# Kernel optimization log

Measured on AMD Instinct MI355X. Metric: run time of the kernel, lower is better.

## Reference

```python
import jax, jax.numpy as jnp
import numpy as np

B = 1024      # batch
D = 512       # input/output dim per module
H = 1024      # expert hidden dim
T = 8         # num_tasks
NTE = 2       # experts per task
NSE = 2       # shared experts
E = T * NTE + NSE   # 18 experts per layer
# expert_input_idx: each expert reads the module it belongs to (tasks 0..7, shared=8)
EXPERT_IDX = np.array([m for m in range(T + 1) for _ in range(2)])  # [E]


def _lin_init(k, shape, fan_in):
    s = 1.0 / np.sqrt(fan_in)
    return jax.random.uniform(k, shape, jnp.float32, -s, s)


def setup_inputs() -> dict:
    key = jax.random.key(0)
    ks = jax.random.split(key, 20)
    inp = {"inputs": jax.random.normal(ks[0], (B, T + 1, D), jnp.float32)}
    # layer 0: experts D->H->D (stacked over E), gates for M=9 modules
    inp["W1_0"] = _lin_init(ks[1], (E, D, H), D)
    inp["b1_0"] = _lin_init(ks[2], (E, H), D)
    inp["W2_0"] = _lin_init(ks[3], (E, H, D), H)
    inp["b2_0"] = _lin_init(ks[4], (E, D), H)
    inp["Wg_0"] = _lin_init(ks[5], (T + 1, D, E), D)
    inp["bg_0"] = _lin_init(ks[6], (T + 1, E), D)
    # layer 1 (final): gates only for M=T modules
    inp["W1_1"] = _lin_init(ks[7], (E, D, H), D)
    inp["b1_1"] = _lin_init(ks[8], (E, H), D)
    inp["W2_1"] = _lin_init(ks[9], (E, H, D), H)
    inp["b2_1"] = _lin_init(ks[10], (E, D), H)
    inp["Wg_1"] = _lin_init(ks[11], (T, D, E), D)
    inp["bg_1"] = _lin_init(ks[12], (T, E), D)
    # self-exp residual weights: per task [L=2, NTE], shared [L-1=1, NSE]
    sc = 1.0 / np.sqrt(NTE)
    inp["sew_task"] = jax.random.uniform(ks[13], (T, 2, NTE), jnp.float32, -sc, sc)
    inp["sew_shared"] = jax.random.uniform(ks[14], (1, NSE), jnp.float32, -sc, sc)
    return inp


def _build_add(rows):
    # rows: list of [2]-vectors, one per fully-active module; block-diagonal layout
    M = len(rows)
    add = jnp.zeros((M, E), jnp.float32)
    for m, w in enumerate(rows):
        add = add.at[m, 2 * m:2 * m + 2].set(w)
    return add


def _layer(x, W1, b1, W2, b2, Wg, bg, add):
    # x: [B, M_in, D]; experts share input of their owning module
    xe = x[:, EXPERT_IDX, :]                                   # [B, E, D]
    h = jax.nn.relu(jnp.einsum('bed,edh->beh', xe, W1) + b1)   # [B, E, H]
    eo = jnp.einsum('beh,eho->beo', h, W2) + b2                # [B, E, D]
    M = Wg.shape[0]
    g = jax.nn.softmax(jnp.einsum('bmd,mde->bme', x[:, :M, :], Wg) + bg, axis=-1)
    g = g + add[None]                                          # self-exp residual
    return jnp.einsum('bme,beo->bmo', g, eo)                   # [B, M, D]


def reference(inputs, W1_0, b1_0, W2_0, b2_0, Wg_0, bg_0,
              W1_1, b1_1, W2_1, b2_1, Wg_1, bg_1, sew_task, sew_shared):
    add0 = _build_add([sew_task[t, 0] for t in range(T)] + [sew_shared[0]])  # [T+1, E]
    add1 = _build_add([sew_task[t, 1] for t in range(T)])                    # [T, E]
    x = _layer(inputs, W1_0, b1_0, W2_0, b2_0, Wg_0, bg_0, add0)  # [B, T+1, D]
    x = _layer(x, W1_1, b1_1, W2_1, b2_1, Wg_1, bg_1, add1)       # [B, T, D]
    return x
```

## Files before the change

kernel.cpp:

```cpp
#include <hip/hip_runtime.h>

typedef unsigned short u16;
typedef unsigned int u32;
typedef __attribute__((ext_vector_type(8))) short short8;
typedef __attribute__((ext_vector_type(4))) float floatx4;

#define GLOAD_LDS16(gp, lp)                                                              \
  __builtin_amdgcn_global_load_lds((const __attribute__((address_space(1))) void*)(gp),  \
                                   (__attribute__((address_space(3))) void*)(lp), 16, 0, 0)

__device__ __forceinline__ u16 f2bf(float f) {
  u32 u = __float_as_uint(f);
  u += 0x7fffu + ((u >> 16) & 1u);
  return (u16)(u >> 16);
}

__device__ __forceinline__ void bf8_to_f(const u16* p, float* o) {
  const uint4 v = *(const uint4*)p;
  const u32 a[4] = {v.x, v.y, v.z, v.w};
#pragma unroll
  for (int i = 0; i < 4; i++) {
    o[2 * i]     = __uint_as_float(a[i] << 16);
    o[2 * i + 1] = __uint_as_float(a[i] & 0xffff0000u);
  }
}

__global__ __launch_bounds__(256) void prep_kernel(
    const float* __restrict__ W1a, const float* __restrict__ W2a,
    const float* __restrict__ W1b, const float* __restrict__ W2b,
    u16* __restrict__ T1a, u16* __restrict__ T2a,
    u16* __restrict__ T1b, u16* __restrict__ T2b,
    const float* __restrict__ Wg0, const float* __restrict__ Wg1,
    u16* __restrict__ WgT0, u16* __restrict__ WgT1,
    const float* __restrict__ x0, u16* __restrict__ x0bf) {
  __shared__ float tile[64][65];
  const int id = blockIdx.x;
  const int t = threadIdx.x;

  if (id < 9216) {
    const int tsel = id / 2304;
    const int rem = id % 2304;
    const int e = rem >> 7;
    const int t128 = rem & 127;
    const int K = (tsel & 1) ? 1024 : 512;
    const int N = (tsel & 1) ? 512 : 1024;
    const int kt = (tsel & 1) ? (t128 & 15) : (t128 & 7);
    const int nt = (tsel & 1) ? (t128 >> 4) : (t128 >> 3);
    const int k0 = kt * 64, n0 = nt * 64;
    const float* W = (tsel == 0) ? W1a : (tsel == 1) ? W2a : (tsel == 2) ? W1b : W2b;
    u16* WT = (tsel == 0) ? T1a : (tsel == 1) ? T2a : (tsel == 2) ? T1b : T2b;

    const float* Wp = W + ((size_t)e * K + k0) * N + n0;
    const int r = t >> 4;
    const int c = (t & 15) << 2;
#pragma unroll
    for (int p = 0; p < 4; p++) {
      const int row = r + p * 16;
      const float4 v = *(const float4*)(Wp + (size_t)row * N + c);
      tile[row][c + 0] = v.x; tile[row][c + 1] = v.y;
      tile[row][c + 2] = v.z; tile[row][c + 3] = v.w;
    }
    __syncthreads();
    u16* WTp = WT + ((size_t)e * N + n0) * K + k0;
#pragma unroll
    for (int p = 0; p < 4; p++) {
      const int row = r + p * 16;
      u32 lo = (u32)f2bf(tile[c + 0][row]) | ((u32)f2bf(tile[c + 1][row]) << 16);
      u32 hi = (u32)f2bf(tile[c + 2][row]) | ((u32)f2bf(tile[c + 3][row]) << 16);
      *(uint2*)(WTp + (size_t)row * K + c) = make_uint2(lo, hi);
    }
  } else if (id < 9828) {
    int idx = (id - 9216) * 256 + t;
    const float* Wg = Wg0;
    u16* WgT = WgT0;
    if (idx >= 82944) { idx -= 82944; Wg = Wg1; WgT = WgT1; }
    const int d = idx & 511;
    const int r = idx >> 9;
    const int e = r % 18;
    const int m = r / 18;
    WgT[idx] = f2bf(Wg[((size_t)(m * 512 + d)) * 18 + e]);
  } else {
    const int i = (id - 9828) * 256 + t;
    const float4 v = ((const float4*)x0)[i];
    u32 lo = (u32)f2bf(v.x) | ((u32)f2bf(v.y) << 16);
    u32 hi = (u32)f2bf(v.z) | ((u32)f2bf(v.w) << 16);
    ((uint2*)x0bf)[i] = make_uint2(lo, hi);
  }
}

template <int M, int LAYER>
__device__ __forceinline__ void gating_body(
    int bid, const u16* __restrict__ xbf, const u16* __restrict__ WgT,
    const float* __restrict__ bg, const float* __restrict__ sew_task,
    const float* __restrict__ sew_shared, float* __restrict__ wsm) {
  const int lane = threadIdx.x & 63;
  const int wave = threadIdx.x >> 6;
  const int m = bid >> 7;
  const int b0 = (bid & 127) * 8 + wave * 2;

  float xa[8], xb[8];
  bf8_to_f(xbf + (size_t)b0 * 4608 + m * 512 + lane * 8, xa);
  bf8_to_f(xbf + (size_t)(b0 + 1) * 4608 + m * 512 + lane * 8, xb);

  float lg0[18], lg1[18];
#pragma unroll
  for (int e = 0; e < 18; e++) {
    float w[8];
    bf8_to_f(WgT + ((size_t)m * 18 + e) * 512 + lane * 8, w);
    float s0 = 0.f, s1 = 0.f;
#pragma unroll
    for (int i = 0; i < 8; i++) { s0 = fmaf(w[i], xa[i], s0); s1 = fmaf(w[i], xb[i], s1); }
#pragma unroll
    for (int off = 1; off < 64; off <<= 1) {
      s0 += __shfl_xor(s0, off, 64);
      s1 += __shfl_xor(s1, off, 64);
    }
    const float bgv = bg[m * 18 + e];
    lg0[e] = s0 + bgv;
    lg1[e] = s1 + bgv;
  }
  float mx0 = lg0[0], mx1 = lg1[0];
#pragma unroll
  for (int e = 1; e < 18; e++) { mx0 = fmaxf(mx0, lg0[e]); mx1 = fmaxf(mx1, lg1[e]); }
  float sum0 = 0.f, sum1 = 0.f;
#pragma unroll
  for (int e = 0; e < 18; e++) { sum0 += __expf(lg0[e] - mx0); sum1 += __expf(lg1[e] - mx1); }
  float my0 = lg0[0], my1 = lg1[0];
#pragma unroll
  for (int e = 1; e < 18; e++)
    if (lane == e) { my0 = lg0[e]; my1 = lg1[e]; }
  float w0 = __expf(my0 - mx0) / sum0;
  float w1 = __expf(my1 - mx1) / sum1;
  if ((lane >> 1) == m) {
    float add;
    if (M == 9 && m == 8) add = sew_shared[lane & 1];
    else                  add = sew_task[m * 4 + 2 * LAYER + (lane & 1)];
    w0 += add; w1 += add;
  }
  if (lane < 18) {
    wsm[((size_t)b0 * M + m) * 18 + lane] = w0;
    wsm[((size_t)(b0 + 1) * M + m) * 18 + lane] = w1;
  }
}

template <bool RELU_BF16_OUT, int M, int LAYER, bool GATE>
__global__ __launch_bounds__(256, 3) void gemm_fused_kernel(
    const u16* __restrict__ A, const u16* __restrict__ BT,
    const float* __restrict__ bias, void* __restrict__ Cout,
    int lda, int a_shift, int a_mul, int ldc, int c_mul, int N, int K, int nshift, int G,
    const u16* __restrict__ WgT, const float* __restrict__ bg,
    const float* __restrict__ sewt, const float* __restrict__ sews,
    float* __restrict__ wsm) {
  if (GATE && (int)blockIdx.x >= G) {
    gating_body<M, LAYER>(blockIdx.x - G, A, WgT, bg, sewt, sews, wsm);
    return;
  }
  __shared__ __align__(16) u16 As[128 * 64];
  __shared__ __align__(16) u16 Bs[128 * 64];

  const int tid = threadIdx.x;
  const int lane = tid & 63;
  const int wave = tid >> 6;

  const int L = blockIdx.x;
  const int per_xcd = G >> 3;
  const int g = (L & 7) * per_xcd + (L >> 3);
  const int e = g >> nshift;
  const int wb = g & ((1 << nshift) - 1);
  const int mt = wb & 7;
  const int nt = wb >> 3;
  const int m0 = mt << 7, n0 = nt << 7;

  const u16* Aexp = A + (size_t)((e >> a_shift) * a_mul);
  const u16* Bexp = BT + (size_t)e * (size_t)N * (size_t)K;

  const int colsw = (((lane & 7) ^ ((lane >> 3) & 7)) << 3);
  const u16* aptr[4];
  const u16* bptr[4];
  u16* lA[4];
  u16* lB[4];
#pragma unroll
  for (int i = 0; i < 4; i++) {
    const int cch = wave * 4 + i;
    const int row = cch * 8 + (lane >> 3);
    aptr[i] = Aexp + (size_t)(m0 + row) * lda + colsw;
    bptr[i] = Bexp + (size_t)(n0 + row) * K + colsw;
    lA[i] = As + cch * 512;
    lB[i] = Bs + cch * 512;
  }

  floatx4 acc[4][4];
#pragma unroll
  for (int i = 0; i < 4; i++)
#pragma unroll
    for (int j = 0; j < 4; j++) acc[i][j] = (floatx4){0.f, 0.f, 0.f, 0.f};

  const int wm = (wave & 1) << 6;
  const int wn = (wave >> 1) << 6;
  const int r15 = lane & 15;
  const int quad = lane >> 4;

  int aoff[4], boff[4];
#pragma unroll
  for (int i = 0; i < 4; i++) {
    const int ra = wm + i * 16 + r15;
    aoff[i] = ra * 64 + ((quad ^ (ra & 7)) << 3);
    const int rb = wn + i * 16 + r15;
    boff[i] = rb * 64 + ((quad ^ (rb & 7)) << 3);
  }

  for (int k0 = 0; k0 < K; k0 += 64) {
    __syncthreads();
#pragma unroll
    for (int i = 0; i < 4; i++) GLOAD_LDS16(aptr[i] + k0, lA[i]);
#pragma unroll
    for (int i = 0; i < 4; i++) GLOAD_LDS16(bptr[i] + k0, lB[i]);
    __syncthreads();
#pragma unroll
    for (int s = 0; s < 2; s++) {
      short8 af[4], bfr[4];
#pragma unroll
      for (int i = 0; i < 4; i++) af[i] = *(const short8*)(As + (aoff[i] ^ (s << 5)));
#pragma unroll
      for (int j = 0; j < 4; j++) bfr[j] = *(const short8*)(Bs + (boff[j] ^ (s << 5)));
#pragma unroll
      for (int i = 0; i < 4; i++)
#pragma unroll
        for (int j = 0; j < 4; j++)
          acc[i][j] = __builtin_amdgcn_mfma_f32_16x16x32_bf16(af[i], bfr[j], acc[i][j], 0, 0, 0);
    }
  }

  const int ccol0 = n0 + wn + r15;
  const int crow0 = m0 + wm + quad * 4;
  float bv[4];
#pragma unroll
  for (int j = 0; j < 4; j++) bv[j] = bias[e * N + ccol0 + j * 16];

  if constexpr (RELU_BF16_OUT) {
    u16* Co = (u16*)Cout + (size_t)e * c_mul;
#pragma unroll
    for (int i = 0; i < 4; i++)
#pragma unroll
      for (int r = 0; r < 4; r++) {
        const size_t rowoff = (size_t)(crow0 + i * 16 + r) * ldc;
#pragma unroll
        for (int j = 0; j < 4; j++) {
          float v = acc[i][j][r] + bv[j];
          v = v > 0.f ? v : 0.f;
          Co[rowoff + ccol0 + j * 16] = f2bf(v);
        }
      }
  } else {
    float* Co = (float*)Cout + (size_t)e * c_mul;
#pragma unroll
    for (int i = 0; i < 4; i++)
#pragma unroll
      for (int r = 0; r < 4; r++) {
        const size_t rowoff = (size_t)(crow0 + i * 16 + r) * ldc;
#pragma unroll
        for (int j = 0; j < 4; j++) Co[rowoff + ccol0 + j * 16] = acc[i][j][r] + bv[j];
      }
  }
}

template <int M, bool BF16OUT>
__global__ __launch_bounds__(256) void wsum_kernel(
    const float* __restrict__ eo, const float* __restrict__ wsm,
    float* __restrict__ outf, u16* __restrict__ outb) {
  __shared__ float ws[2 * M * 18];
  const int t = threadIdx.x;
  const int b0 = blockIdx.x * 2;
  for (int i = t; i < 2 * M * 18; i += 256) ws[i] = wsm[(size_t)b0 * M * 18 + i];
  __syncthreads();
  const int lb = t >> 7;
  const int s = t & 127;
  const int b = b0 + lb;
  const float* eob = eo + (size_t)b * 9216 + s * 4;
  const float* wr = ws + lb * M * 18;

  float4 acc[M];
#pragma unroll
  for (int m = 0; m < M; m++) acc[m] = make_float4(0.f, 0.f, 0.f, 0.f);
#pragma unroll
  for (int e = 0; e < 18; e++) {
    const float4 v = *(const float4*)(eob + e * 512);
#pragma unroll
    for (int m = 0; m < M; m++) {
      const float w = wr[m * 18 + e];
      acc[m].x = fmaf(w, v.x, acc[m].x);
      acc[m].y = fmaf(w, v.y, acc[m].y);
      acc[m].z = fmaf(w, v.z, acc[m].z);
      acc[m].w = fmaf(w, v.w, acc[m].w);
    }
  }
  if constexpr (BF16OUT) {
    u16* ob = outb + (size_t)b * 4608 + s * 4;
#pragma unroll
    for (int m = 0; m < M; m++) {
      u32 lo = (u32)f2bf(acc[m].x) | ((u32)f2bf(acc[m].y) << 16);
      u32 hi = (u32)f2bf(acc[m].z) | ((u32)f2bf(acc[m].w) << 16);
      *(uint2*)(ob + m * 512) = make_uint2(lo, hi);
    }
  } else {
    float* ob = outf + (size_t)b * (M * 512) + s * 4;
#pragma unroll
    for (int m = 0; m < M; m++) *(float4*)(ob + m * 512) = acc[m];
  }
}

extern "C" void kernel_launch(void* const* d_in, const int* in_sizes, int n_in,
                              void* d_out, int out_size, void* d_ws, size_t ws_size,
                              hipStream_t stream) {
  const float* x0   = (const float*)d_in[0];
  const float* W1_0 = (const float*)d_in[1];
  const float* b1_0 = (const float*)d_in[2];
  const float* W2_0 = (const float*)d_in[3];
  const float* b2_0 = (const float*)d_in[4];
  const float* Wg_0 = (const float*)d_in[5];
  const float* bg_0 = (const float*)d_in[6];
  const float* W1_1 = (const float*)d_in[7];
  const float* b1_1 = (const float*)d_in[8];
  const float* W2_1 = (const float*)d_in[9];
  const float* b2_1 = (const float*)d_in[10];
  const float* Wg_1 = (const float*)d_in[11];
  const float* bg_1 = (const float*)d_in[12];
  const float* sewt = (const float*)d_in[13];
  const float* sews = (const float*)d_in[14];
  float* out = (float*)d_out;

  char* p = (char*)d_ws;
  auto take = [&](size_t n) { char* r = p; p += (n + 255) & ~(size_t)255; return r; };
  u16*   x0bf = (u16*)take(4718592ull * 2);
  u16*   W1T0 = (u16*)take(9437184ull * 2);
  u16*   W2T0 = (u16*)take(9437184ull * 2);
  u16*   W1T1 = (u16*)take(9437184ull * 2);
  u16*   W2T1 = (u16*)take(9437184ull * 2);
  u16*   WgT0 = (u16*)take(82944ull * 2);
  u16*   WgT1 = (u16*)take(73728ull * 2);
  u16*   hbf  = (u16*)take(18874368ull * 2);
  float* eo   = (float*)take(9437184ull * 4);
  u16*   x1bf = (u16*)take(4718592ull * 2);
  float* wsm0 = (float*)take(165888ull * 4);
  float* wsm1 = (float*)take(147456ull * 4);

  dim3 blk(256);
  prep_kernel<<<dim3(14436), blk, 0, stream>>>(W1_0, W2_0, W1_1, W2_1,
                                               W1T0, W2T0, W1T1, W2T1,
                                               Wg_0, Wg_1, WgT0, WgT1, x0, x0bf);
  gemm_fused_kernel<true, 9, 0, true><<<dim3(1152 + 1152), blk, 0, stream>>>(
      x0bf, W1T0, b1_0, (void*)hbf, 4608, 1, 512, 18432, 1024, 1024, 512, 6, 1152,
      WgT0, bg_0, sewt, sews, wsm0);
  gemm_fused_kernel<false, 9, 0, false><<<dim3(576), blk, 0, stream>>>(
      hbf, W2T0, b2_0, (void*)eo, 18432, 0, 1024, 9216, 512, 512, 1024, 5, 576,
      nullptr, nullptr, nullptr, nullptr, nullptr);
  wsum_kernel<9, true><<<dim3(512), blk, 0, stream>>>(eo, wsm0, nullptr, x1bf);
  gemm_fused_kernel<true, 8, 1, true><<<dim3(1152 + 1024), blk, 0, stream>>>(
      x1bf, W1T1, b1_1, (void*)hbf, 4608, 1, 512, 18432, 1024, 1024, 512, 6, 1152,
      WgT1, bg_1, sewt, sews, wsm1);
  gemm_fused_kernel<false, 8, 1, false><<<dim3(576), blk, 0, stream>>>(
      hbf, W2T1, b2_1, (void*)eo, 18432, 0, 1024, 9216, 512, 512, 1024, 5, 576,
      nullptr, nullptr, nullptr, nullptr, nullptr);
  wsum_kernel<8, false><<<dim3(512), blk, 0, stream>>>(eo, wsm1, out, nullptr);
}
```

Baseline: 375.8 us.

## Double-buffer LDS tiles in expert GEMM to overlap global loads with MFMA

```diff
diff --git a/kernel.cpp b/kernel.cpp
--- a/kernel.cpp
+++ b/kernel.cpp
@@ -8,6 +8,8 @@
 #define GLOAD_LDS16(gp, lp)                                                              \
   __builtin_amdgcn_global_load_lds((const __attribute__((address_space(1))) void*)(gp),  \
                                    (__attribute__((address_space(3))) void*)(lp), 16, 0, 0)
+
+#define WAITV0 asm volatile("s_waitcnt vmcnt(0)" ::: "memory")
 
 __device__ __forceinline__ u16 f2bf(float f) {
   u32 u = __float_as_uint(f);
@@ -144,7 +146,7 @@
 }
 
 template <bool RELU_BF16_OUT, int M, int LAYER, bool GATE>
-__global__ __launch_bounds__(256, 3) void gemm_fused_kernel(
+__global__ __launch_bounds__(256, 2) void gemm_fused_kernel(
     const u16* __restrict__ A, const u16* __restrict__ BT,
     const float* __restrict__ bias, void* __restrict__ Cout,
     int lda, int a_shift, int a_mul, int ldc, int c_mul, int N, int K, int nshift, int G,
@@ -155,8 +157,8 @@
     gating_body<M, LAYER>(blockIdx.x - G, A, WgT, bg, sewt, sews, wsm);
     return;
   }
-  __shared__ __align__(16) u16 As[128 * 64];
-  __shared__ __align__(16) u16 Bs[128 * 64];
+  __shared__ __align__(16) u16 As[2 * 128 * 64];
+  __shared__ __align__(16) u16 Bs[2 * 128 * 64];
 
   const int tid = threadIdx.x;
   const int lane = tid & 63;
@@ -209,26 +211,43 @@
     boff[i] = rb * 64 + ((quad ^ (rb & 7)) << 3);
   }
 
-  for (int k0 = 0; k0 < K; k0 += 64) {
-    __syncthreads();
-#pragma unroll
-    for (int i = 0; i < 4; i++) GLOAD_LDS16(aptr[i] + k0, lA[i]);
-#pragma unroll
-    for (int i = 0; i < 4; i++) GLOAD_LDS16(bptr[i] + k0, lB[i]);
-    __syncthreads();
+#pragma unroll
+  for (int i = 0; i < 4; i++) GLOAD_LDS16(aptr[i], lA[i]);
+#pragma unroll
+  for (int i = 0; i < 4; i++) GLOAD_LDS16(bptr[i], lB[i]);
+  WAITV0;
+  __builtin_amdgcn_s_barrier();
+
+  const int NT = K >> 6;
+  for (int kt = 0; kt < NT; kt++) {
+    const int cur = (kt & 1) << 13;
+    const int nxt = cur ^ 8192;
+    if (kt + 1 < NT) {
+      const int k1 = (kt + 1) << 6;
+#pragma unroll
+      for (int i = 0; i < 4; i++) GLOAD_LDS16(aptr[i] + k1, lA[i] + nxt);
+#pragma unroll
+      for (int i = 0; i < 4; i++) GLOAD_LDS16(bptr[i] + k1, lB[i] + nxt);
+    }
+    const u16* Asb = As + cur;
+    const u16* Bsb = Bs + cur;
 #pragma unroll
     for (int s = 0; s < 2; s++) {
       short8 af[4], bfr[4];
 #pragma unroll
-      for (int i = 0; i < 4; i++) af[i] = *(const short8*)(As + (aoff[i] ^ (s << 5)));
-#pragma unroll
-      for (int j = 0; j < 4; j++) bfr[j] = *(const short8*)(Bs + (boff[j] ^ (s << 5)));
+      for (int i = 0; i < 4; i++) af[i] = *(const short8*)(Asb + (aoff[i] ^ (s << 5)));
+#pragma unroll
+      for (int j = 0; j < 4; j++) bfr[j] = *(const short8*)(Bsb + (boff[j] ^ (s << 5)));
+      __builtin_amdgcn_s_setprio(1);
 #pragma unroll
       for (int i = 0; i < 4; i++)
 #pragma unroll
         for (int j = 0; j < 4; j++)
           acc[i][j] = __builtin_amdgcn_mfma_f32_16x16x32_bf16(af[i], bfr[j], acc[i][j], 0, 0, 0);
-    }
+      __builtin_amdgcn_s_setprio(0);
+    }
+    WAITV0;
+    __builtin_amdgcn_s_barrier();
   }
 
   const int ccol0 = n0 + wn + r15;
```

Result: slower. 399.1 us (+6.2%).
